# Kernel optimization log

Hardware: AMD Instinct MI355X
Metric: run time of the kernel (lower is better)

## Reference

```python
import jax, jax.numpy as jnp
import numpy as np


def _rotate_half(x):
    x1, x2 = jnp.split(x, 2, axis=-1)
    return jnp.concatenate([-x2, x1], axis=-1)


def _rope_tables(seq_len, head_dim, base=10000.0):
    inv_freq = 1.0 / (base ** (jnp.arange(0, head_dim, 2, dtype=jnp.float32) / head_dim))
    t = jnp.arange(seq_len, dtype=jnp.float32)
    freqs = jnp.outer(t, inv_freq)  # [S, head_dim/2]
    # torch .repeat(...,2) tiles along last dim -> concat
    cos = jnp.concatenate([jnp.cos(freqs), jnp.cos(freqs)], axis=-1)  # [S, head_dim]
    sin = jnp.concatenate([jnp.sin(freqs), jnp.sin(freqs)], axis=-1)
    return cos[None, None], sin[None, None]  # [1,1,S,head_dim]


def setup_inputs() -> dict:
    key = jax.random.key(0)
    ks = jax.random.split(key, 5)
    B, S, D = 2, 2048, 2048
    sd = 1.0 / np.sqrt(D)
    return {
        "x": jax.random.normal(ks[0], (B, S, D), dtype=jnp.float32),
        "Wq": jax.random.normal(ks[1], (D, D), dtype=jnp.float32) * sd,
        "Wk": jax.random.normal(ks[2], (D, D), dtype=jnp.float32) * sd,
        "Wv": jax.random.normal(ks[3], (D, D), dtype=jnp.float32) * sd,
        "Wo": jax.random.normal(ks[4], (D, D), dtype=jnp.float32) * sd,
        "n_heads": 16,
    }


def reference(x, Wq, Wk, Wv, Wo, n_heads):
    B, S, D = x.shape
    hd = D // n_heads
    # projections (torch Linear: x @ W.T)
    def proj(W):
        return (x @ W.T).reshape(B, S, n_heads, hd).transpose(0, 2, 1, 3)  # [B,H,S,hd]
    q, k, v = proj(Wq), proj(Wk), proj(Wv)
    cos, sin = _rope_tables(S, hd)
    q = q * cos + _rotate_half(q) * sin
    k = k * cos + _rotate_half(k) * sin
    scale = 1.0 / np.sqrt(hd)
    scores = jnp.einsum('bhsd,bhtd->bhst', q, k) * scale  # [B,H,S,S]
    causal = jnp.triu(jnp.ones((S, S), dtype=bool), k=1)
    scores = jnp.where(causal[None, None], -jnp.inf, scores)
    attn = jax.nn.softmax(scores, axis=-1)
    out = jnp.einsum('bhst,bhtd->bhsd', attn, v)
    out = out.transpose(0, 2, 1, 3).reshape(B, S, D)
    return out @ Wo.T
```

## Files before the change

### kernel.cpp

```cpp
#include <hip/hip_runtime.h>
#include <hip/hip_bf16.h>
#include <math.h>

typedef __attribute__((ext_vector_type(8))) short bf16x8;
typedef __attribute__((ext_vector_type(4))) float f32x4;

#define GLB_CAST(p) ((const __attribute__((address_space(1))) void*)(p))
#define LDS_CAST(p) ((__attribute__((address_space(3))) void*)(p))

static __device__ __forceinline__ unsigned short bf16_bits(float x) {
    __hip_bfloat16 h = __float2bfloat16(x);
    return *(unsigned short*)&h;
}

#define QSC 0.127517455f
#define THR_LOG2 11.5415605f

__global__ void cvt_all(const float* __restrict__ x,  const float* __restrict__ wq,
                        const float* __restrict__ wk, const float* __restrict__ wv,
                        const float* __restrict__ wo,
                        __hip_bfloat16* __restrict__ xb,  __hip_bfloat16* __restrict__ wqb,
                        __hip_bfloat16* __restrict__ wkb, __hip_bfloat16* __restrict__ wvb,
                        __hip_bfloat16* __restrict__ wob)
{
    const size_t NX = 8388608, NW = 4194304;
    size_t i = ((size_t)blockIdx.x * 256 + threadIdx.x) * 8;
    const float* s; __hip_bfloat16* d; size_t off;
    if (i < NX) { s = x; d = xb; off = i; }
    else {
        size_t k = i - NX;
        const int seg = (int)(k >> 22);
        off = k & (NW - 1);
        s = seg == 0 ? wq : seg == 1 ? wk : seg == 2 ? wv : wo;
        d = seg == 0 ? wqb : seg == 1 ? wkb : seg == 2 ? wvb : wob;
    }
    float4 a = *(const float4*)(s + off);
    float4 b = *(const float4*)(s + off + 4);
    float t[8] = {a.x, a.y, a.z, a.w, b.x, b.y, b.z, b.w};
    union { unsigned short u[8]; uint4 v; } o;
#pragma unroll
    for (int j = 0; j < 8; ++j) o.u[j] = bf16_bits(t[j]);
    *(uint4*)(d + off) = o.v;
}

__global__ __launch_bounds__(256, 2)
void gemm_qkv(const __hip_bfloat16* __restrict__ A,
              const __hip_bfloat16* __restrict__ Wq,
              const __hip_bfloat16* __restrict__ Wk,
              const __hip_bfloat16* __restrict__ Wv,
              __hip_bfloat16* __restrict__ Qo,
              __hip_bfloat16* __restrict__ Ko,
              __hip_bfloat16* __restrict__ Vto)
{
    const int K = 2048;
    __shared__ __hip_bfloat16 As[128 * 32];
    __shared__ __hip_bfloat16 Bs[128 * 32];
    __shared__ __hip_bfloat16 Ct[128 * 128];
    const int tid = threadIdx.x;
    const int w = tid >> 6, l = tid & 63;
    const int sel = blockIdx.y >> 4;
    const __hip_bfloat16* Bt = sel == 0 ? Wq : (sel == 1 ? Wk : Wv);
    const int m0 = blockIdx.x * 128, n0 = (blockIdx.y & 15) * 128;
    const int wr = w >> 1, wc = w & 1;
    const int lr = l & 15, kh = l >> 4;

    f32x4 acc[4][4] = {};

    for (int kt = 0; kt < 64; ++kt) {
        const int kb = kt * 32;
#pragma unroll
        for (int i = 0; i < 2; ++i) {
            const int s = i * 256 + tid;
            const int r = s >> 2, ks = (s & 3) * 8;
            __builtin_amdgcn_global_load_lds(GLB_CAST(A + (size_t)(m0 + r) * K + kb + ks),
                                             LDS_CAST(As + (size_t)(i * 256 + w * 64) * 8),
                                             16, 0, 0);
            __builtin_amdgcn_global_load_lds(GLB_CAST(Bt + (size_t)(n0 + r) * K + kb + ks),
                                             LDS_CAST(Bs + (size_t)(i * 256 + w * 64) * 8),
                                             16, 0, 0);
        }
        __syncthreads();
        bf16x8 af[4], bfr[4];
#pragma unroll
        for (int m = 0; m < 4; ++m)
            af[m] = *(const bf16x8*)(As + (wr * 64 + m * 16 + lr) * 32 + kh * 8);
#pragma unroll
        for (int n = 0; n < 4; ++n)
            bfr[n] = *(const bf16x8*)(Bs + (wc * 64 + n * 16 + lr) * 32 + kh * 8);
#pragma unroll
        for (int m = 0; m < 4; ++m)
#pragma unroll
            for (int n = 0; n < 4; ++n)
                acc[m][n] = __builtin_amdgcn_mfma_f32_16x16x32_bf16(af[m], bfr[n], acc[m][n], 0, 0, 0);
        __syncthreads();
    }

    const int h = n0 >> 7;
    if (sel < 2) {
        __hip_bfloat16* Cout = sel == 0 ? Qo : Ko;
        const float osc = (sel == 0) ? QSC : 1.0f;
#pragma unroll
        for (int m = 0; m < 4; ++m)
#pragma unroll
            for (int n = 0; n < 4; ++n)
#pragma unroll
                for (int j = 0; j < 4; ++j)
                    Ct[(wr * 64 + m * 16 + kh * 4 + j) * 128 + wc * 64 + n * 16 + lr] =
                        __float2bfloat16(acc[m][n][j]);
        __syncthreads();
        float inv_n[4];
#pragma unroll
        for (int n = 0; n < 4; ++n) {
            const int c = wc * 64 + n * 16 + lr;
            inv_n[n] = __expf((float)(c & 63) * (-0.14391156831212787f));
        }
#pragma unroll
        for (int m = 0; m < 4; ++m) {
#pragma unroll
            for (int j = 0; j < 4; ++j) {
                const int rl = wr * 64 + m * 16 + kh * 4 + j;
                const int r = m0 + rl;
                const int b = r >> 11, sy = r & 2047;
                const float fs = (float)sy;
#pragma unroll
                for (int n = 0; n < 4; ++n) {
                    const int c = wc * 64 + n * 16 + lr;
                    float sn, cs;
                    __sincosf(fs * inv_n[n], &sn, &cs);
                    const float own = acc[m][n][j];
                    const float partner = __bfloat162float(Ct[rl * 128 + (c ^ 64)]);
                    const float outv = (c < 64) ? own * cs - partner * sn
                                                : own * cs + partner * sn;
                    Cout[((size_t)(b * 16 + h) * 2048 + sy) * 128 + c] =
                        __float2bfloat16(outv * osc);
                }
            }
        }
    } else {
#pragma unroll
        for (int m = 0; m < 4; ++m) {
            const int r0 = m0 + wr * 64 + m * 16 + kh * 4;
#pragma unroll
            for (int n = 0; n < 4; ++n) {
                const int c = wc * 64 + n * 16 + lr;
#pragma unroll
                for (int j = 0; j < 4; ++j) {
                    const int r = r0 + j;
                    const int b = r >> 11, sy = r & 2047;
                    Vto[((size_t)(b * 16 + h) * 128 + c) * 2048 + sy] =
                        __float2bfloat16(acc[m][n][j]);
                }
            }
        }
    }
}

__global__ __launch_bounds__(256, 2)
void gemm_o(const __hip_bfloat16* __restrict__ A,
            const __hip_bfloat16* __restrict__ Bt,
            float* __restrict__ Cout)
{
    const int K = 2048;
    __shared__ __hip_bfloat16 As[128 * 32];
    __shared__ __hip_bfloat16 Bs[128 * 32];
    const int tid = threadIdx.x;
    const int w = tid >> 6, l = tid & 63;
    const int m0 = blockIdx.x * 128, n0 = blockIdx.y * 128;
    const int wr = w >> 1, wc = w & 1;
    const int lr = l & 15, kh = l >> 4;

    f32x4 acc[4][4] = {};

    for (int kt = 0; kt < 64; ++kt) {
        const int kb = kt * 32;
#pragma unroll
        for (int i = 0; i < 2; ++i) {
            const int s = i * 256 + tid;
            const int r = s >> 2, ks = (s & 3) * 8;
            __builtin_amdgcn_global_load_lds(GLB_CAST(A + (size_t)(m0 + r) * K + kb + ks),
                                             LDS_CAST(As + (size_t)(i * 256 + w * 64) * 8),
                                             16, 0, 0);
            __builtin_amdgcn_global_load_lds(GLB_CAST(Bt + (size_t)(n0 + r) * K + kb + ks),
                                             LDS_CAST(Bs + (size_t)(i * 256 + w * 64) * 8),
                                             16, 0, 0);
        }
        __syncthreads();
        bf16x8 af[4], bfr[4];
#pragma unroll
        for (int m = 0; m < 4; ++m)
            af[m] = *(const bf16x8*)(As + (wr * 64 + m * 16 + lr) * 32 + kh * 8);
#pragma unroll
        for (int n = 0; n < 4; ++n)
            bfr[n] = *(const bf16x8*)(Bs + (wc * 64 + n * 16 + lr) * 32 + kh * 8);
#pragma unroll
        for (int m = 0; m < 4; ++m)
#pragma unroll
            for (int n = 0; n < 4; ++n)
                acc[m][n] = __builtin_amdgcn_mfma_f32_16x16x32_bf16(af[m], bfr[n], acc[m][n], 0, 0, 0);
        __syncthreads();
    }

#pragma unroll
    for (int m = 0; m < 4; ++m) {
        const int r0 = m0 + wr * 64 + m * 16 + kh * 4;
#pragma unroll
        for (int n = 0; n < 4; ++n) {
            const int c = n0 + wc * 64 + n * 16 + lr;
#pragma unroll
            for (int j = 0; j < 4; ++j)
                Cout[(size_t)(r0 + j) * 2048 + c] = acc[m][n][j];
        }
    }
}

__global__ __launch_bounds__(256, 3)
void flash_part(const __hip_bfloat16* __restrict__ Q,
                const __hip_bfloat16* __restrict__ K,
                const __hip_bfloat16* __restrict__ Vt,
                __hip_bfloat16* __restrict__ AO,
                __hip_bfloat16* __restrict__ OP,
                float* __restrict__ ML)
{
    const int bh = blockIdx.x;
    const int u  = blockIdx.y;
    const int tid = threadIdx.x, w = tid >> 6, l = tid & 63;
    const int lr = l & 15, hi = l >> 4;

    int G, part, P;
    if (u < 16)      { G = 12 + (u >> 2);            part = u & 3;   P = 4; }
    else if (u < 28) { int v = u - 16; G = 8 + v / 3; part = v % 3;  P = 3; }
    else if (u < 36) { int v = u - 28; G = 4 + (v >> 1); part = v & 1; P = 2; }
    else             { G = u - 36;                   part = 0;       P = 1; }
    const int nt = 4 * G + 4;
    const int t0 = (part * nt) / P, t1 = ((part + 1) * nt) / P;
    const bool split = (P > 1);
    const int qb = G * 128 + w * 32;
    const int q0 = qb + lr, q1 = qb + 16 + lr;

    const __hip_bfloat16* Qb = Q  + (size_t)bh * 2048 * 128;
    const __hip_bfloat16* Kb = K  + (size_t)bh * 2048 * 128;
    const __hip_bfloat16* Vb = Vt + (size_t)bh * 128 * 2048;

    __shared__ __align__(16) __hip_bfloat16 Ks[2][32 * 128];
    __shared__ __align__(16) __hip_bfloat16 Vs[2][128 * 32];

    bf16x8 qf[2][4];
#pragma unroll
    for (int g = 0; g < 2; ++g)
#pragma unroll
        for (int kk = 0; kk < 4; ++kk)
            qf[g][kk] = *(const bf16x8*)(Qb + (size_t)(qb + g * 16 + lr) * 128 + kk * 32 + hi * 8);

    int rK[2], cK[2], rV[2], cV[2];
#pragma unroll
    for (int i = 0; i < 2; ++i) {
        const int ci = i * 4 + w;
        rK[i] = ci * 4 + (l >> 4);
        cK[i] = ((l & 15) ^ (rK[i] & 7)) * 8;
        rV[i] = ci * 16 + (l >> 2);
        cV[i] = ((l & 3) ^ (rV[i] & 3)) * 8;
    }
    const int rsw7 = lr & 7, vsw3 = lr & 3;
    const int sA = lr + ((hi & 1) << 5);
    const int sB = sA + 16;
    const bool plo = (hi < 2);

#define STAGE(buf, t)                                                                        \
    {                                                                                        \
        const int kv0_ = (t) * 32;                                                           \
        _Pragma("unroll")                                                                    \
        for (int i = 0; i < 2; ++i) {                                                        \
            __builtin_amdgcn_global_load_lds(                                                \
                GLB_CAST(Kb + (size_t)(kv0_ + rK[i]) * 128 + cK[i]),                         \
                LDS_CAST(&Ks[buf][(i * 4 + w) * 512]), 16, 0, 0);                            \
            __builtin_amdgcn_global_load_lds(                                                \
                GLB_CAST(Vb + (size_t)rV[i] * 2048 + kv0_ + cV[i]),                          \
                LDS_CAST(&Vs[buf][(i * 4 + w) * 512]), 16, 0, 0);                            \
        }                                                                                    \
    }

    f32x4 o[2][8] = {};
    float mrow[2] = {-1e30f, -1e30f};
    float lrow[2] = {0.f, 0.f};

    int cur = 0;
    STAGE(0, t0);
    __syncthreads();

    for (int t = t0; t < t1; ++t) {
        if (t + 1 < t1) STAGE(cur ^ 1, t + 1);
        const __hip_bfloat16* Kc = &Ks[cur][0];
        const __hip_bfloat16* Vc = &Vs[cur][0];
        const int kv0 = t * 32;

        f32x4 sT[2][2] = {};
#pragma unroll
        for (int f = 0; f < 2; ++f)
#pragma unroll
            for (int kk = 0; kk < 4; ++kk) {
                const bf16x8 kf = *(const bf16x8*)(Kc + (f * 16 + lr) * 128 +
                                                   ((kk * 4 + hi) ^ rsw7) * 8);
                sT[0][f] = __builtin_amdgcn_mfma_f32_16x16x32_bf16(kf, qf[0][kk], sT[0][f], 0, 0, 0);
                sT[1][f] = __builtin_amdgcn_mfma_f32_16x16x32_bf16(kf, qf[1][kk], sT[1][f], 0, 0, 0);
            }

        if (kv0 + 31 > qb) {
#pragma unroll
            for (int g = 0; g < 2; ++g) {
                const int qown = g ? q1 : q0;
#pragma unroll
                for (int f = 0; f < 2; ++f)
#pragma unroll
                    for (int j = 0; j < 4; ++j) {
                        const int kv = kv0 + f * 16 + hi * 4 + j;
                        if (kv > qown) sT[g][f][j] = -1e30f;
                    }
            }
        }

        float pmax[2];
#pragma unroll
        for (int g = 0; g < 2; ++g) {
            float mx = sT[g][0][0];
#pragma unroll
            for (int f = 0; f < 2; ++f)
#pragma unroll
                for (int j = 0; j < 4; ++j) mx = fmaxf(mx, sT[g][f][j]);
            mx = fmaxf(mx, __shfl_xor(mx, 16));
            mx = fmaxf(mx, __shfl_xor(mx, 32));
            pmax[g] = mx;
        }

        if (!__all(pmax[0] <= mrow[0] + THR_LOG2 && pmax[1] <= mrow[1] + THR_LOG2)) {
#pragma unroll
            for (int g = 0; g < 2; ++g) {
                const float mnew = fmaxf(mrow[g], pmax[g]);
                const float alpha = exp2f(mrow[g] - mnew);
                mrow[g] = mnew;
                lrow[g] *= alpha;
                float aj[4];
#pragma unroll
                for (int j = 0; j < 4; ++j)
                    aj[j] = __shfl(alpha, (l & 48) | (hi * 4 + j), 64);
#pragma unroll
                for (int dn = 0; dn < 8; ++dn)
#pragma unroll
                    for (int j = 0; j < 4; ++j) o[g][dn][j] *= aj[j];
            }
        }

#pragma unroll
        for (int g = 0; g < 2; ++g) {
            float rs = 0.f;
#pragma unroll
            for (int f = 0; f < 2; ++f)
#pragma unroll
                for (int j = 0; j < 4; ++j) {
                    const float pv = exp2f(sT[g][f][j] - mrow[g]);
                    sT[g][f][j] = pv;
                    rs += pv;
                }
            rs += __shfl_xor(rs, 16);
            rs += __shfl_xor(rs, 32);
            lrow[g] += rs;
        }

        union { unsigned u[4]; bf16x8 v; } pf[2];
#pragma unroll
        for (int g = 0; g < 2; ++g) {
            unsigned wds[4];
#pragma unroll
            for (int i = 0; i < 4; ++i)
                wds[i] = (unsigned)bf16_bits(sT[g][i >> 1][(i & 1) * 2]) |
                         ((unsigned)bf16_bits(sT[g][i >> 1][(i & 1) * 2 + 1]) << 16);
            const unsigned a0 = __shfl((int)wds[0], sA, 64), a1 = __shfl((int)wds[1], sA, 64);
            const unsigned a2 = __shfl((int)wds[2], sA, 64), a3 = __shfl((int)wds[3], sA, 64);
            const unsigned b0 = __shfl((int)wds[0], sB, 64), b1 = __shfl((int)wds[1], sB, 64);
            const unsigned b2 = __shfl((int)wds[2], sB, 64), b3 = __shfl((int)wds[3], sB, 64);
            pf[g].u[0] = plo ? a0 : a2;
            pf[g].u[1] = plo ? a1 : a3;
            pf[g].u[2] = plo ? b0 : b2;
            pf[g].u[3] = plo ? b1 : b3;
        }

#pragma unroll
        for (int dn = 0; dn < 8; ++dn) {
            const bf16x8 vf = *(const bf16x8*)(Vc + (dn * 16 + lr) * 32 + (hi ^ vsw3) * 8);
            o[0][dn] = __builtin_amdgcn_mfma_f32_16x16x32_bf16(pf[0].v, vf, o[0][dn], 0, 0, 0);
            o[1][dn] = __builtin_amdgcn_mfma_f32_16x16x32_bf16(pf[1].v, vf, o[1][dn], 0, 0, 0);
        }
        __syncthreads();
        cur ^= 1;
    }
#undef STAGE

    if (!split) {
#pragma unroll
        for (int g = 0; g < 2; ++g) {
            float linv[4];
#pragma unroll
            for (int j = 0; j < 4; ++j)
                linv[j] = 1.0f / __shfl(lrow[g], (l & 48) | (hi * 4 + j), 64);
#pragma unroll
            for (int j = 0; j < 4; ++j) {
                const int q = qb + g * 16 + hi * 4 + j;
                const size_t rb = ((size_t)(bh >> 4) * 2048 + q) * 2048 + (size_t)(bh & 15) * 128;
#pragma unroll
                for (int dn = 0; dn < 8; ++dn)
                    AO[rb + dn * 16 + lr] = __float2bfloat16(o[g][dn][j] * linv[j]);
            }
        }
    } else {
        const int base = (G < 8) ? (G - 4) * 2 : ((G < 12) ? 8 + (G - 8) * 3
                                                           : 20 + (G - 12) * 4);
        const int pidx = bh * 36 + base + part;
#pragma unroll
        for (int g = 0; g < 2; ++g) {
#pragma unroll
            for (int j = 0; j < 4; ++j) {
                const int row = w * 32 + g * 16 + hi * 4 + j;
#pragma unroll
                for (int dn = 0; dn < 8; ++dn)
                    OP[((size_t)pidx * 128 + row) * 128 + dn * 16 + lr] =
                        __float2bfloat16(o[g][dn][j]);
            }
            if (l < 16) {
                const int row = w * 32 + g * 16 + l;
                ML[((size_t)pidx * 128 + row) * 2]     = mrow[g];
                ML[((size_t)pidx * 128 + row) * 2 + 1] = lrow[g];
            }
        }
    }
}

__global__ void flash_merge(const __hip_bfloat16* __restrict__ OP,
                            const float* __restrict__ ML,
                            __hip_bfloat16* __restrict__ AO)
{
    const int gi = blockIdx.x % 12, bh = blockIdx.x / 12;
    const int G = 4 + gi;
    const int P = (G < 8) ? 2 : ((G < 12) ? 3 : 4);
    const int base = (G < 8) ? (G - 4) * 2 : ((G < 12) ? 8 + (G - 8) * 3
                                                       : 20 + (G - 12) * 4);
    const int pidx0 = bh * 36 + base;
    const int t = threadIdx.x, r = t >> 1, c0 = (t & 1) * 64;

    float m[4], lv[4];
    float M = -1e30f;
#pragma unroll
    for (int p = 0; p < 4; ++p) if (p < P) {
        m[p]  = ML[((size_t)(pidx0 + p) * 128 + r) * 2];
        lv[p] = ML[((size_t)(pidx0 + p) * 128 + r) * 2 + 1];
        M = fmaxf(M, m[p]);
    }
    float wgt[4];
    float den = 0.f;
#pragma unroll
    for (int p = 0; p < 4; ++p) if (p < P) {
        wgt[p] = exp2f(m[p] - M);
        den += lv[p] * wgt[p];
    }
    const float inv = 1.0f / den;

    const int q = G * 128 + r;
    __hip_bfloat16* out = AO + ((size_t)(bh >> 4) * 2048 + q) * 2048 + (size_t)(bh & 15) * 128 + c0;

#pragma unroll
    for (int ch = 0; ch < 8; ++ch) {
        float acc[8] = {0.f, 0.f, 0.f, 0.f, 0.f, 0.f, 0.f, 0.f};
#pragma unroll
        for (int p = 0; p < 4; ++p) if (p < P) {
            const bf16x8 v = *(const bf16x8*)(OP + ((size_t)(pidx0 + p) * 128 + r) * 128 + c0 + ch * 8);
#pragma unroll
            for (int i = 0; i < 8; ++i) {
                __hip_bfloat16 hv;
                *(short*)&hv = v[i];
                acc[i] += __bfloat162float(hv) * wgt[p];
            }
        }
        union { unsigned short us[8]; bf16x8 v; } rr;
#pragma unroll
        for (int i = 0; i < 8; ++i) rr.us[i] = bf16_bits(acc[i] * inv);
        *(bf16x8*)(out + ch * 8) = rr.v;
    }
}

extern "C" void kernel_launch(void* const* d_in, const int* in_sizes, int n_in,
                              void* d_out, int out_size, void* d_ws, size_t ws_size,
                              hipStream_t stream) {
    (void)in_sizes; (void)n_in; (void)out_size; (void)ws_size;
    const float* x  = (const float*)d_in[0];
    const float* Wq = (const float*)d_in[1];
    const float* Wk = (const float*)d_in[2];
    const float* Wv = (const float*)d_in[3];
    const float* Wo = (const float*)d_in[4];

    char* p = (char*)d_ws;
    auto carve = [&](size_t bytes) -> char* {
        char* r = p;
        p += (bytes + 255) & ~(size_t)255;
        return r;
    };
    __hip_bfloat16* xb  = (__hip_bfloat16*)carve(4096ull * 2048 * 2);
    __hip_bfloat16* Wqb = (__hip_bfloat16*)carve(2048ull * 2048 * 2);
    __hip_bfloat16* Wkb = (__hip_bfloat16*)carve(2048ull * 2048 * 2);
    __hip_bfloat16* Wvb = (__hip_bfloat16*)carve(2048ull * 2048 * 2);
    __hip_bfloat16* Wob = (__hip_bfloat16*)carve(2048ull * 2048 * 2);
    __hip_bfloat16* Qb  = (__hip_bfloat16*)carve(32ull * 2048 * 128 * 2);
    __hip_bfloat16* Kb  = (__hip_bfloat16*)carve(32ull * 2048 * 128 * 2);
    __hip_bfloat16* Vtb = (__hip_bfloat16*)carve(32ull * 128 * 2048 * 2);
    __hip_bfloat16* OPb = (__hip_bfloat16*)carve(32ull * 36 * 128 * 128 * 2);
    float*          MLb = (float*)carve(32ull * 36 * 128 * 2 * 4);

    cvt_all<<<12288, 256, 0, stream>>>(x, Wq, Wk, Wv, Wo, xb, Wqb, Wkb, Wvb, Wob);

    gemm_qkv<<<dim3(32, 48), 256, 0, stream>>>(xb, Wqb, Wkb, Wvb, Qb, Kb, Vtb);

    flash_part<<<dim3(32, 40), 256, 0, stream>>>(Qb, Kb, Vtb, xb , OPb, MLb);
    flash_merge<<<384, 256, 0, stream>>>(OPb, MLb, xb );

    gemm_o<<<dim3(32, 16), 256, 0, stream>>>(xb, Wob, (float*)d_out);
}
```

Baseline: 293.0 us.

## Restructure flash attention to 8 waves with 16 query rows and 64-wide KV tiles

The flash attention kernel now runs 512 threads per block, with each wave owning 16 query rows instead of 32, and stages 64-row K/V tiles per iteration instead of 32. This halves per-wave accumulator registers and halves the number of loop iterations and barriers, with larger LDS buffers and a new V swizzle. It also raises wave priority around the MFMA sections with s_setprio. The cost is more LDS per block, which may lower block occupancy, and each K/V tile is now shared by more waves.

```diff
diff --git a/kernel.cpp b/kernel.cpp
--- a/kernel.cpp
+++ b/kernel.cpp
@@ -213,7 +213,7 @@
     }
 }
 
-__global__ __launch_bounds__(256, 3)
+__global__ __launch_bounds__(512, 4)
 void flash_part(const __hip_bfloat16* __restrict__ Q,
                 const __hip_bfloat16* __restrict__ K,
                 const __hip_bfloat16* __restrict__ Vt,
@@ -231,57 +231,54 @@
     else if (u < 28) { int v = u - 16; G = 8 + v / 3; part = v % 3;  P = 3; }
     else if (u < 36) { int v = u - 28; G = 4 + (v >> 1); part = v & 1; P = 2; }
     else             { G = u - 36;                   part = 0;       P = 1; }
-    const int nt = 4 * G + 4;
+    const int nt = 2 * G + 2;
     const int t0 = (part * nt) / P, t1 = ((part + 1) * nt) / P;
     const bool split = (P > 1);
-    const int qb = G * 128 + w * 32;
-    const int q0 = qb + lr, q1 = qb + 16 + lr;
+    const int qb = G * 128 + w * 16;
+    const int q0 = qb + lr;
 
     const __hip_bfloat16* Qb = Q  + (size_t)bh * 2048 * 128;
     const __hip_bfloat16* Kb = K  + (size_t)bh * 2048 * 128;
     const __hip_bfloat16* Vb = Vt + (size_t)bh * 128 * 2048;
 
-    __shared__ __align__(16) __hip_bfloat16 Ks[2][32 * 128];
-    __shared__ __align__(16) __hip_bfloat16 Vs[2][128 * 32];
-
-    bf16x8 qf[2][4];
-#pragma unroll
-    for (int g = 0; g < 2; ++g)
-#pragma unroll
-        for (int kk = 0; kk < 4; ++kk)
-            qf[g][kk] = *(const bf16x8*)(Qb + (size_t)(qb + g * 16 + lr) * 128 + kk * 32 + hi * 8);
+    __shared__ __align__(16) __hip_bfloat16 Ks[2][64 * 128];
+    __shared__ __align__(16) __hip_bfloat16 Vs[2][128 * 64];
+
+    bf16x8 qf[4];
+#pragma unroll
+    for (int kk = 0; kk < 4; ++kk)
+        qf[kk] = *(const bf16x8*)(Qb + (size_t)(qb + lr) * 128 + kk * 32 + hi * 8);
 
     int rK[2], cK[2], rV[2], cV[2];
 #pragma unroll
     for (int i = 0; i < 2; ++i) {
-        const int ci = i * 4 + w;
-        rK[i] = ci * 4 + (l >> 4);
-        cK[i] = ((l & 15) ^ (rK[i] & 7)) * 8;
-        rV[i] = ci * 16 + (l >> 2);
-        cV[i] = ((l & 3) ^ (rV[i] & 3)) * 8;
-    }
-    const int rsw7 = lr & 7, vsw3 = lr & 3;
+        const int slot = i * 512 + tid;
+        rK[i] = slot >> 4;
+        cK[i] = ((slot & 15) ^ (rK[i] & 7)) * 8;
+        rV[i] = slot >> 3;
+        cV[i] = ((slot & 7) ^ (rV[i] & 7)) * 8;
+    }
+    const int rsw7 = lr & 7;
     const int sA = lr + ((hi & 1) << 5);
     const int sB = sA + 16;
-    const bool plo = (hi < 2);
+    const bool hsel = (hi >> 1) != 0;
 
 #define STAGE(buf, t)                                                                        \
     {                                                                                        \
-        const int kv0_ = (t) * 32;                                                           \
+        const int kv0_ = (t) * 64;                                                           \
         _Pragma("unroll")                                                                    \
         for (int i = 0; i < 2; ++i) {                                                        \
             __builtin_amdgcn_global_load_lds(                                                \
                 GLB_CAST(Kb + (size_t)(kv0_ + rK[i]) * 128 + cK[i]),                         \
-                LDS_CAST(&Ks[buf][(i * 4 + w) * 512]), 16, 0, 0);                            \
+                LDS_CAST(&Ks[buf][(i * 8 + w) * 512]), 16, 0, 0);                            \
             __builtin_amdgcn_global_load_lds(                                                \
                 GLB_CAST(Vb + (size_t)rV[i] * 2048 + kv0_ + cV[i]),                          \
-                LDS_CAST(&Vs[buf][(i * 4 + w) * 512]), 16, 0, 0);                            \
+                LDS_CAST(&Vs[buf][(i * 8 + w) * 512]), 16, 0, 0);                            \
         }                                                                                    \
     }
 
-    f32x4 o[2][8] = {};
-    float mrow[2] = {-1e30f, -1e30f};
-    float lrow[2] = {0.f, 0.f};
+    f32x4 o[8] = {};
+    float mrow = -1e30f, lrow = 0.f;
 
     int cur = 0;
     STAGE(0, t0);
@@ -291,144 +288,135 @@
         if (t + 1 < t1) STAGE(cur ^ 1, t + 1);
         const __hip_bfloat16* Kc = &Ks[cur][0];
         const __hip_bfloat16* Vc = &Vs[cur][0];
-        const int kv0 = t * 32;
-
-        f32x4 sT[2][2] = {};
-#pragma unroll
-        for (int f = 0; f < 2; ++f)
+        const int kv0 = t * 64;
+
+        f32x4 sT[4] = {};
+        __builtin_amdgcn_s_setprio(1);
+#pragma unroll
+        for (int f = 0; f < 4; ++f)
 #pragma unroll
             for (int kk = 0; kk < 4; ++kk) {
                 const bf16x8 kf = *(const bf16x8*)(Kc + (f * 16 + lr) * 128 +
                                                    ((kk * 4 + hi) ^ rsw7) * 8);
-                sT[0][f] = __builtin_amdgcn_mfma_f32_16x16x32_bf16(kf, qf[0][kk], sT[0][f], 0, 0, 0);
-                sT[1][f] = __builtin_amdgcn_mfma_f32_16x16x32_bf16(kf, qf[1][kk], sT[1][f], 0, 0, 0);
+                sT[f] = __builtin_amdgcn_mfma_f32_16x16x32_bf16(kf, qf[kk], sT[f], 0, 0, 0);
             }
-
-        if (kv0 + 31 > qb) {
-#pragma unroll
-            for (int g = 0; g < 2; ++g) {
-                const int qown = g ? q1 : q0;
-#pragma unroll
-                for (int f = 0; f < 2; ++f)
-#pragma unroll
-                    for (int j = 0; j < 4; ++j) {
-                        const int kv = kv0 + f * 16 + hi * 4 + j;
-                        if (kv > qown) sT[g][f][j] = -1e30f;
-                    }
+        __builtin_amdgcn_s_setprio(0);
+
+        if (kv0 + 63 > qb) {
+#pragma unroll
+            for (int f = 0; f < 4; ++f)
+#pragma unroll
+                for (int j = 0; j < 4; ++j) {
+                    const int kv = kv0 + f * 16 + hi * 4 + j;
+                    if (kv > q0) sT[f][j] = -1e30f;
+                }
+        }
+
+        float pmax = sT[0][0];
+#pragma unroll
+        for (int f = 0; f < 4; ++f)
+#pragma unroll
+            for (int j = 0; j < 4; ++j) pmax = fmaxf(pmax, sT[f][j]);
+        pmax = fmaxf(pmax, __shfl_xor(pmax, 16));
+        pmax = fmaxf(pmax, __shfl_xor(pmax, 32));
+
+        if (!__all(pmax <= mrow + THR_LOG2)) {
+            const float mnew = fmaxf(mrow, pmax);
+            const float alpha = exp2f(mrow - mnew);
+            mrow = mnew;
+            lrow *= alpha;
+            float aj[4];
+#pragma unroll
+            for (int j = 0; j < 4; ++j)
+                aj[j] = __shfl(alpha, (l & 48) | (hi * 4 + j), 64);
+#pragma unroll
+            for (int dn = 0; dn < 8; ++dn)
+#pragma unroll
+                for (int j = 0; j < 4; ++j) o[dn][j] *= aj[j];
+        }
+
+        float rs = 0.f;
+#pragma unroll
+        for (int f = 0; f < 4; ++f)
+#pragma unroll
+            for (int j = 0; j < 4; ++j) {
+                const float pv = exp2f(sT[f][j] - mrow);
+                sT[f][j] = pv;
+                rs += pv;
             }
-        }
-
-        float pmax[2];
-#pragma unroll
-        for (int g = 0; g < 2; ++g) {
-            float mx = sT[g][0][0];
-#pragma unroll
-            for (int f = 0; f < 2; ++f)
-#pragma unroll
-                for (int j = 0; j < 4; ++j) mx = fmaxf(mx, sT[g][f][j]);
-            mx = fmaxf(mx, __shfl_xor(mx, 16));
-            mx = fmaxf(mx, __shfl_xor(mx, 32));
-            pmax[g] = mx;
-        }
-
-        if (!__all(pmax[0] <= mrow[0] + THR_LOG2 && pmax[1] <= mrow[1] + THR_LOG2)) {
-#pragma unroll
-            for (int g = 0; g < 2; ++g) {
-                const float mnew = fmaxf(mrow[g], pmax[g]);
-                const float alpha = exp2f(mrow[g] - mnew);
-                mrow[g] = mnew;
-                lrow[g] *= alpha;
-                float aj[4];
-#pragma unroll
-                for (int j = 0; j < 4; ++j)
-                    aj[j] = __shfl(alpha, (l & 48) | (hi * 4 + j), 64);
-#pragma unroll
-                for (int dn = 0; dn < 8; ++dn)
-#pragma unroll
-                    for (int j = 0; j < 4; ++j) o[g][dn][j] *= aj[j];
-            }
-        }
-
-#pragma unroll
-        for (int g = 0; g < 2; ++g) {
-            float rs = 0.f;
-#pragma unroll
-            for (int f = 0; f < 2; ++f)
-#pragma unroll
-                for (int j = 0; j < 4; ++j) {
-                    const float pv = exp2f(sT[g][f][j] - mrow[g]);
-                    sT[g][f][j] = pv;
-                    rs += pv;
-                }
-            rs += __shfl_xor(rs, 16);
-            rs += __shfl_xor(rs, 32);
-            lrow[g] += rs;
-        }
-
-        union { unsigned u[4]; bf16x8 v; } pf[2];
-#pragma unroll
-        for (int g = 0; g < 2; ++g) {
-            unsigned wds[4];
-#pragma unroll
-            for (int i = 0; i < 4; ++i)
-                wds[i] = (unsigned)bf16_bits(sT[g][i >> 1][(i & 1) * 2]) |
-                         ((unsigned)bf16_bits(sT[g][i >> 1][(i & 1) * 2 + 1]) << 16);
-            const unsigned a0 = __shfl((int)wds[0], sA, 64), a1 = __shfl((int)wds[1], sA, 64);
-            const unsigned a2 = __shfl((int)wds[2], sA, 64), a3 = __shfl((int)wds[3], sA, 64);
-            const unsigned b0 = __shfl((int)wds[0], sB, 64), b1 = __shfl((int)wds[1], sB, 64);
-            const unsigned b2 = __shfl((int)wds[2], sB, 64), b3 = __shfl((int)wds[3], sB, 64);
-            pf[g].u[0] = plo ? a0 : a2;
-            pf[g].u[1] = plo ? a1 : a3;
-            pf[g].u[2] = plo ? b0 : b2;
-            pf[g].u[3] = plo ? b1 : b3;
-        }
-
+        rs += __shfl_xor(rs, 16);
+        rs += __shfl_xor(rs, 32);
+        lrow += rs;
+
+        unsigned wds[8];
+#pragma unroll
+        for (int f = 0; f < 4; ++f)
+#pragma unroll
+            for (int hh = 0; hh < 2; ++hh)
+                wds[f * 2 + hh] = (unsigned)bf16_bits(sT[f][hh * 2]) |
+                                  ((unsigned)bf16_bits(sT[f][hh * 2 + 1]) << 16);
+
+        unsigned av[8], bv[8];
+#pragma unroll
+        for (int i = 0; i < 8; ++i) {
+            av[i] = __shfl((int)wds[i], sA, 64);
+            bv[i] = __shfl((int)wds[i], sB, 64);
+        }
+        union { unsigned u[4]; bf16x8 v; } pa[2];
+        pa[0].u[0] = hsel ? av[2] : av[0];
+        pa[0].u[1] = hsel ? av[3] : av[1];
+        pa[0].u[2] = hsel ? bv[2] : bv[0];
+        pa[0].u[3] = hsel ? bv[3] : bv[1];
+        pa[1].u[0] = hsel ? av[6] : av[4];
+        pa[1].u[1] = hsel ? av[7] : av[5];
+        pa[1].u[2] = hsel ? bv[6] : bv[4];
+        pa[1].u[3] = hsel ? bv[7] : bv[5];
+
+        __builtin_amdgcn_s_setprio(1);
 #pragma unroll
         for (int dn = 0; dn < 8; ++dn) {
-            const bf16x8 vf = *(const bf16x8*)(Vc + (dn * 16 + lr) * 32 + (hi ^ vsw3) * 8);
-            o[0][dn] = __builtin_amdgcn_mfma_f32_16x16x32_bf16(pf[0].v, vf, o[0][dn], 0, 0, 0);
-            o[1][dn] = __builtin_amdgcn_mfma_f32_16x16x32_bf16(pf[1].v, vf, o[1][dn], 0, 0, 0);
-        }
+            const int vrow = (dn * 16 + lr) * 64;
+            const bf16x8 vf0 = *(const bf16x8*)(Vc + vrow + ((0 + hi) ^ rsw7) * 8);
+            const bf16x8 vf1 = *(const bf16x8*)(Vc + vrow + ((4 + hi) ^ rsw7) * 8);
+            o[dn] = __builtin_amdgcn_mfma_f32_16x16x32_bf16(pa[0].v, vf0, o[dn], 0, 0, 0);
+            o[dn] = __builtin_amdgcn_mfma_f32_16x16x32_bf16(pa[1].v, vf1, o[dn], 0, 0, 0);
+        }
+        __builtin_amdgcn_s_setprio(0);
+
         __syncthreads();
         cur ^= 1;
     }
 #undef STAGE
 
     if (!split) {
-#pragma unroll
-        for (int g = 0; g < 2; ++g) {
-            float linv[4];
-#pragma unroll
-            for (int j = 0; j < 4; ++j)
-                linv[j] = 1.0f / __shfl(lrow[g], (l & 48) | (hi * 4 + j), 64);
-#pragma unroll
-            for (int j = 0; j < 4; ++j) {
-                const int q = qb + g * 16 + hi * 4 + j;
-                const size_t rb = ((size_t)(bh >> 4) * 2048 + q) * 2048 + (size_t)(bh & 15) * 128;
-#pragma unroll
-                for (int dn = 0; dn < 8; ++dn)
-                    AO[rb + dn * 16 + lr] = __float2bfloat16(o[g][dn][j] * linv[j]);
-            }
+        float linv[4];
+#pragma unroll
+        for (int j = 0; j < 4; ++j)
+            linv[j] = 1.0f / __shfl(lrow, (l & 48) | (hi * 4 + j), 64);
+#pragma unroll
+        for (int j = 0; j < 4; ++j) {
+            const int q = qb + hi * 4 + j;
+            const size_t rb = ((size_t)(bh >> 4) * 2048 + q) * 2048 + (size_t)(bh & 15) * 128;
+#pragma unroll
+            for (int dn = 0; dn < 8; ++dn)
+                AO[rb + dn * 16 + lr] = __float2bfloat16(o[dn][j] * linv[j]);
         }
     } else {
         const int base = (G < 8) ? (G - 4) * 2 : ((G < 12) ? 8 + (G - 8) * 3
                                                            : 20 + (G - 12) * 4);
         const int pidx = bh * 36 + base + part;
 #pragma unroll
-        for (int g = 0; g < 2; ++g) {
-#pragma unroll
-            for (int j = 0; j < 4; ++j) {
-                const int row = w * 32 + g * 16 + hi * 4 + j;
-#pragma unroll
-                for (int dn = 0; dn < 8; ++dn)
-                    OP[((size_t)pidx * 128 + row) * 128 + dn * 16 + lr] =
-                        __float2bfloat16(o[g][dn][j]);
-            }
-            if (l < 16) {
-                const int row = w * 32 + g * 16 + l;
-                ML[((size_t)pidx * 128 + row) * 2]     = mrow[g];
-                ML[((size_t)pidx * 128 + row) * 2 + 1] = lrow[g];
-            }
+        for (int j = 0; j < 4; ++j) {
+            const int row = w * 16 + hi * 4 + j;
+#pragma unroll
+            for (int dn = 0; dn < 8; ++dn)
+                OP[((size_t)pidx * 128 + row) * 128 + dn * 16 + lr] =
+                    __float2bfloat16(o[dn][j]);
+        }
+        if (l < 16) {
+            const int row = w * 16 + l;
+            ML[((size_t)pidx * 128 + row) * 2]     = mrow;
+            ML[((size_t)pidx * 128 + row) * 2 + 1] = lrow;
         }
     }
 }
@@ -516,7 +504,7 @@
 
     gemm_qkv<<<dim3(32, 48), 256, 0, stream>>>(xb, Wqb, Wkb, Wvb, Qb, Kb, Vtb);
 
-    flash_part<<<dim3(32, 40), 256, 0, stream>>>(Qb, Kb, Vtb, xb , OPb, MLb);
+    flash_part<<<dim3(32, 40), 512, 0, stream>>>(Qb, Kb, Vtb, xb , OPb, MLb);
     flash_merge<<<384, 256, 0, stream>>>(OPb, MLb, xb );
 
     gemm_o<<<dim3(32, 16), 256, 0, stream>>>(xb, Wob, (float*)d_out);
```

Result: no change. 287.8 us (-1.8%).

## Double KV tile to 64 per iteration in flash attention and add MFMA priority hints

Applied to the files above, without the earlier changes.

Each flash-attention iteration now processes a 64-key tile instead of 32. The K/V LDS buffers double in size, the staging loads and swizzles are reworked for 64-wide V rows, and the P fragment packing produces two k-halves for the PV MFMAs. This halves the number of loop iterations, barriers and softmax rescale steps per block. s_setprio hints are added around the MFMA sections. In exchange it uses more LDS and registers, so launch bounds drop to 2 blocks per SIMD, which lowers occupancy. It also wastes more masked work on diagonal tiles.

```diff
diff --git a/kernel.cpp b/kernel.cpp
--- a/kernel.cpp
+++ b/kernel.cpp
@@ -213,7 +213,7 @@
     }
 }
 
-__global__ __launch_bounds__(256, 3)
+__global__ __launch_bounds__(256, 2)
 void flash_part(const __hip_bfloat16* __restrict__ Q,
                 const __hip_bfloat16* __restrict__ K,
                 const __hip_bfloat16* __restrict__ Vt,
@@ -231,7 +231,7 @@
     else if (u < 28) { int v = u - 16; G = 8 + v / 3; part = v % 3;  P = 3; }
     else if (u < 36) { int v = u - 28; G = 4 + (v >> 1); part = v & 1; P = 2; }
     else             { G = u - 36;                   part = 0;       P = 1; }
-    const int nt = 4 * G + 4;
+    const int nt = 2 * G + 2;
     const int t0 = (part * nt) / P, t1 = ((part + 1) * nt) / P;
     const bool split = (P > 1);
     const int qb = G * 128 + w * 32;
@@ -241,8 +241,8 @@
     const __hip_bfloat16* Kb = K  + (size_t)bh * 2048 * 128;
     const __hip_bfloat16* Vb = Vt + (size_t)bh * 128 * 2048;
 
-    __shared__ __align__(16) __hip_bfloat16 Ks[2][32 * 128];
-    __shared__ __align__(16) __hip_bfloat16 Vs[2][128 * 32];
+    __shared__ __align__(16) __hip_bfloat16 Ks[2][64 * 128];
+    __shared__ __align__(16) __hip_bfloat16 Vs[2][128 * 64];
 
     bf16x8 qf[2][4];
 #pragma unroll
@@ -251,25 +251,25 @@
         for (int kk = 0; kk < 4; ++kk)
             qf[g][kk] = *(const bf16x8*)(Qb + (size_t)(qb + g * 16 + lr) * 128 + kk * 32 + hi * 8);
 
-    int rK[2], cK[2], rV[2], cV[2];
-#pragma unroll
-    for (int i = 0; i < 2; ++i) {
-        const int ci = i * 4 + w;
-        rK[i] = ci * 4 + (l >> 4);
-        cK[i] = ((l & 15) ^ (rK[i] & 7)) * 8;
-        rV[i] = ci * 16 + (l >> 2);
-        cV[i] = ((l & 3) ^ (rV[i] & 3)) * 8;
-    }
-    const int rsw7 = lr & 7, vsw3 = lr & 3;
+    int rK[4], cK[4], rV[4], cV[4];
+#pragma unroll
+    for (int i = 0; i < 4; ++i) {
+        const int slot = (i * 4 + w) * 64 + l;
+        rK[i] = slot >> 4;
+        cK[i] = ((slot & 15) ^ (rK[i] & 7)) * 8;
+        rV[i] = slot >> 3;
+        cV[i] = ((slot & 7) ^ (rV[i] & 7)) * 8;
+    }
+    const int rsw7 = lr & 7;
     const int sA = lr + ((hi & 1) << 5);
     const int sB = sA + 16;
-    const bool plo = (hi < 2);
+    const bool hsel = (hi >> 1) != 0;
 
 #define STAGE(buf, t)                                                                        \
     {                                                                                        \
-        const int kv0_ = (t) * 32;                                                           \
+        const int kv0_ = (t) * 64;                                                           \
         _Pragma("unroll")                                                                    \
-        for (int i = 0; i < 2; ++i) {                                                        \
+        for (int i = 0; i < 4; ++i) {                                                        \
             __builtin_amdgcn_global_load_lds(                                                \
                 GLB_CAST(Kb + (size_t)(kv0_ + rK[i]) * 128 + cK[i]),                         \
                 LDS_CAST(&Ks[buf][(i * 4 + w) * 512]), 16, 0, 0);                            \
@@ -291,11 +291,12 @@
         if (t + 1 < t1) STAGE(cur ^ 1, t + 1);
         const __hip_bfloat16* Kc = &Ks[cur][0];
         const __hip_bfloat16* Vc = &Vs[cur][0];
-        const int kv0 = t * 32;
-
-        f32x4 sT[2][2] = {};
-#pragma unroll
-        for (int f = 0; f < 2; ++f)
+        const int kv0 = t * 64;
+
+        f32x4 sT[2][4] = {};
+        __builtin_amdgcn_s_setprio(1);
+#pragma unroll
+        for (int f = 0; f < 4; ++f)
 #pragma unroll
             for (int kk = 0; kk < 4; ++kk) {
                 const bf16x8 kf = *(const bf16x8*)(Kc + (f * 16 + lr) * 128 +
@@ -303,13 +304,14 @@
                 sT[0][f] = __builtin_amdgcn_mfma_f32_16x16x32_bf16(kf, qf[0][kk], sT[0][f], 0, 0, 0);
                 sT[1][f] = __builtin_amdgcn_mfma_f32_16x16x32_bf16(kf, qf[1][kk], sT[1][f], 0, 0, 0);
             }
-
-        if (kv0 + 31 > qb) {
+        __builtin_amdgcn_s_setprio(0);
+
+        if (kv0 + 63 > qb) {
 #pragma unroll
             for (int g = 0; g < 2; ++g) {
                 const int qown = g ? q1 : q0;
 #pragma unroll
-                for (int f = 0; f < 2; ++f)
+                for (int f = 0; f < 4; ++f)
 #pragma unroll
                     for (int j = 0; j < 4; ++j) {
                         const int kv = kv0 + f * 16 + hi * 4 + j;
@@ -323,7 +325,7 @@
         for (int g = 0; g < 2; ++g) {
             float mx = sT[g][0][0];
 #pragma unroll
-            for (int f = 0; f < 2; ++f)
+            for (int f = 0; f < 4; ++f)
 #pragma unroll
                 for (int j = 0; j < 4; ++j) mx = fmaxf(mx, sT[g][f][j]);
             mx = fmaxf(mx, __shfl_xor(mx, 16));
@@ -349,11 +351,12 @@
             }
         }
 
+        union { unsigned u[4]; bf16x8 v; } pa[2][2];
 #pragma unroll
         for (int g = 0; g < 2; ++g) {
             float rs = 0.f;
 #pragma unroll
-            for (int f = 0; f < 2; ++f)
+            for (int f = 0; f < 4; ++f)
 #pragma unroll
                 for (int j = 0; j < 4; ++j) {
                     const float pv = exp2f(sT[g][f][j] - mrow[g]);
@@ -363,32 +366,43 @@
             rs += __shfl_xor(rs, 16);
             rs += __shfl_xor(rs, 32);
             lrow[g] += rs;
-        }
-
-        union { unsigned u[4]; bf16x8 v; } pf[2];
-#pragma unroll
-        for (int g = 0; g < 2; ++g) {
-            unsigned wds[4];
-#pragma unroll
-            for (int i = 0; i < 4; ++i)
-                wds[i] = (unsigned)bf16_bits(sT[g][i >> 1][(i & 1) * 2]) |
-                         ((unsigned)bf16_bits(sT[g][i >> 1][(i & 1) * 2 + 1]) << 16);
-            const unsigned a0 = __shfl((int)wds[0], sA, 64), a1 = __shfl((int)wds[1], sA, 64);
-            const unsigned a2 = __shfl((int)wds[2], sA, 64), a3 = __shfl((int)wds[3], sA, 64);
-            const unsigned b0 = __shfl((int)wds[0], sB, 64), b1 = __shfl((int)wds[1], sB, 64);
-            const unsigned b2 = __shfl((int)wds[2], sB, 64), b3 = __shfl((int)wds[3], sB, 64);
-            pf[g].u[0] = plo ? a0 : a2;
-            pf[g].u[1] = plo ? a1 : a3;
-            pf[g].u[2] = plo ? b0 : b2;
-            pf[g].u[3] = plo ? b1 : b3;
-        }
-
+
+            unsigned wds[8];
+#pragma unroll
+            for (int f = 0; f < 4; ++f)
+#pragma unroll
+                for (int hh = 0; hh < 2; ++hh)
+                    wds[f * 2 + hh] = (unsigned)bf16_bits(sT[g][f][hh * 2]) |
+                                      ((unsigned)bf16_bits(sT[g][f][hh * 2 + 1]) << 16);
+            unsigned av[8], bv[8];
+#pragma unroll
+            for (int i = 0; i < 8; ++i) {
+                av[i] = __shfl((int)wds[i], sA, 64);
+                bv[i] = __shfl((int)wds[i], sB, 64);
+            }
+            pa[g][0].u[0] = hsel ? av[2] : av[0];
+            pa[g][0].u[1] = hsel ? av[3] : av[1];
+            pa[g][0].u[2] = hsel ? bv[2] : bv[0];
+            pa[g][0].u[3] = hsel ? bv[3] : bv[1];
+            pa[g][1].u[0] = hsel ? av[6] : av[4];
+            pa[g][1].u[1] = hsel ? av[7] : av[5];
+            pa[g][1].u[2] = hsel ? bv[6] : bv[4];
+            pa[g][1].u[3] = hsel ? bv[7] : bv[5];
+        }
+
+        __builtin_amdgcn_s_setprio(1);
 #pragma unroll
         for (int dn = 0; dn < 8; ++dn) {
-            const bf16x8 vf = *(const bf16x8*)(Vc + (dn * 16 + lr) * 32 + (hi ^ vsw3) * 8);
-            o[0][dn] = __builtin_amdgcn_mfma_f32_16x16x32_bf16(pf[0].v, vf, o[0][dn], 0, 0, 0);
-            o[1][dn] = __builtin_amdgcn_mfma_f32_16x16x32_bf16(pf[1].v, vf, o[1][dn], 0, 0, 0);
-        }
+            const int vrow = (dn * 16 + lr) * 64;
+            const bf16x8 vf0 = *(const bf16x8*)(Vc + vrow + ((0 + hi) ^ rsw7) * 8);
+            const bf16x8 vf1 = *(const bf16x8*)(Vc + vrow + ((4 + hi) ^ rsw7) * 8);
+            o[0][dn] = __builtin_amdgcn_mfma_f32_16x16x32_bf16(pa[0][0].v, vf0, o[0][dn], 0, 0, 0);
+            o[1][dn] = __builtin_amdgcn_mfma_f32_16x16x32_bf16(pa[1][0].v, vf0, o[1][dn], 0, 0, 0);
+            o[0][dn] = __builtin_amdgcn_mfma_f32_16x16x32_bf16(pa[0][1].v, vf1, o[0][dn], 0, 0, 0);
+            o[1][dn] = __builtin_amdgcn_mfma_f32_16x16x32_bf16(pa[1][1].v, vf1, o[1][dn], 0, 0, 0);
+        }
+        __builtin_amdgcn_s_setprio(0);
+
         __syncthreads();
         cur ^= 1;
     }
```

Measured after the change: 286.7 us (median of 2 runs). 2.1% less time.
